# Kernel optimization log

Hardware: AMD Instinct MI355X
Metric: run time of the kernel (lower is better)

## Reference

```python
import jax, jax.numpy as jnp
import numpy as np

DPSI_THRESHOLD = 0.05
MSE_WEIGHT = 10.0
LOGIT_EPS = 1e-7
N = 8192


def setup_inputs() -> dict:
    key = jax.random.key(0)
    k1, k2 = jax.random.split(key)
    pred_psi_val = jax.random.normal(k1, (N,), dtype=jnp.float32)
    psi_val = jax.random.uniform(k2, (N,), dtype=jnp.float32)
    return {"pred_psi_val": pred_psi_val, "psi_val": psi_val, "use_BCE_loss_only": 0}


def _bce_with_logits(logits, targets):
    # numerically stable BCE-with-logits, mean reduction
    return jnp.mean(jnp.maximum(logits, 0.0) - logits * targets
                    + jnp.log1p(jnp.exp(-jnp.abs(logits))))


def _logit(p, eps):
    # torch.special.logit(p, eps): clamp p to [eps, 1-eps] then log(p/(1-p))
    p = jnp.clip(p, eps, 1.0 - eps)
    return jnp.log(p) - jnp.log1p(-p)


def reference(pred_psi_val, psi_val, use_BCE_loss_only):
    loss = _bce_with_logits(pred_psi_val, psi_val)
    if use_BCE_loss_only:  # static python flag
        return loss
    psi_logit = _logit(psi_val, LOGIT_EPS)
    # all-pairs differences [N, N]
    pred_diff = pred_psi_val[:, None] - pred_psi_val[None, :]
    true_diff = psi_logit[:, None] - psi_logit[None, :]
    ori_true_diff = psi_val[:, None] - psi_val[None, :]
    valid = jnp.abs(ori_true_diff) >= DPSI_THRESHOLD
    n_valid = jnp.sum(valid)
    sq = jnp.where(valid, (pred_diff - true_diff) ** 2, 0.0)
    pairwise_mse = jnp.sum(sq) / jnp.maximum(n_valid, 1).astype(sq.dtype)
    # add pairwise term only if at least one valid pair exists
    return jnp.where(n_valid > 0, loss + MSE_WEIGHT * pairwise_mse, loss)
```

## Files before the change

kernel.cpp:

```cpp
#include <hip/hip_runtime.h>


constexpr float DPSI_T    = 0.05f;
constexpr float LOGIT_EPS = 1e-7f;
constexpr int   CB  = 128;
constexpr int   RPT = 4;
constexpr int   TPB = 256;

__device__ __forceinline__ float logit_f(float p) {
    p = fminf(fmaxf(p, LOGIT_EPS), 1.0f - LOGIT_EPS);
    return logf(p) - log1pf(-p);
}

__global__ __launch_bounds__(256) void pair_kernel(const float* __restrict__ pred,
                                                   const float* __restrict__ psi,
                                                   float* __restrict__ part_sum,
                                                   unsigned int* __restrict__ part_cnt,
                                                   float* __restrict__ part_bce,
                                                   int n) {
    __shared__ float2 tile[CB];
    const int tid = threadIdx.x;
    const float NANF = __int_as_float(0x7fc00000);
    const int slot = blockIdx.x * gridDim.y + blockIdx.y;

    if (tid < CB) {
        int j = blockIdx.y * CB + tid;
        if (j < n) {
            float pj = psi[j];
            tile[tid] = make_float2(pj, pred[j] - logit_f(pj));
        } else {
            tile[tid] = make_float2(NANF, 0.0f);
        }
    }

    float bce = 0.0f;
    if (tid < 16) {
        int i = slot * 16 + tid;
        if (i < n) {
            float x = pred[i], t = psi[i];
            bce = fmaxf(x, 0.0f) - x * t + log1pf(expf(-fabsf(x)));
        }
    }

    float psi_i[RPT], d_i[RPT];
    const int rbase = blockIdx.x * (TPB * RPT);
    #pragma unroll
    for (int r = 0; r < RPT; ++r) {
        int i = rbase + r * TPB + tid;
        if (i < n) {
            float pi = psi[i];
            psi_i[r] = pi;
            d_i[r]   = pred[i] - logit_f(pi);
        } else {
            psi_i[r] = NANF;
            d_i[r]   = 0.0f;
        }
    }
    __syncthreads();

    float sum[RPT] = {0.0f, 0.0f, 0.0f, 0.0f};
    unsigned int cntw = 0;
    #pragma unroll 8
    for (int k = 0; k < CB; ++k) {
        float2 t = tile[k];
        #pragma unroll
        for (int r = 0; r < RPT; ++r) {
            float dpsi = psi_i[r] - t.x;
            bool  v    = fabsf(dpsi) >= DPSI_T;
            float dd   = d_i[r] - t.y;
            float ddm  = v ? dd : 0.0f;
            sum[r] = fmaf(ddm, ddm, sum[r]);
            cntw += (unsigned int)__popcll(__ballot(v));
        }
    }

    float s = (sum[0] + sum[1]) + (sum[2] + sum[3]);
    for (int off = 32; off; off >>= 1) {
        s   += __shfl_down(s, off);
        bce += __shfl_down(bce, off);
    }

    __shared__ float wsum[4];
    __shared__ unsigned int wcnt[4];
    int wave = tid >> 6, lane = tid & 63;
    if (lane == 0) { wsum[wave] = s; wcnt[wave] = cntw; }
    __syncthreads();
    if (tid == 0) {
        float st = (wsum[0] + wsum[1]) + (wsum[2] + wsum[3]);
        unsigned int ct = wcnt[0] + wcnt[1] + wcnt[2] + wcnt[3];
        part_sum[slot] = st;
        part_cnt[slot] = ct;
        part_bce[slot] = bce;
    }
}

__global__ __launch_bounds__(256) void finalize_kernel(const int* __restrict__ flag,
                                                       const float* __restrict__ part_sum,
                                                       const unsigned int* __restrict__ part_cnt,
                                                       const float* __restrict__ part_bce,
                                                       int nparts,
                                                       float* __restrict__ out,
                                                       int n) {
    const int tid = threadIdx.x;

    float s = 0.0f, b = 0.0f;
    unsigned long long c = 0;
    for (int p = tid; p < nparts; p += 256) {
        s += part_sum[p];
        b += part_bce[p];
        c += (unsigned long long)part_cnt[p];
    }

    for (int off = 32; off; off >>= 1) {
        s += __shfl_down(s, off);
        b += __shfl_down(b, off);
        c += __shfl_down(c, off);
    }
    __shared__ float s4[4], b4[4];
    __shared__ unsigned long long c4[4];
    int wave = tid >> 6, lane = tid & 63;
    if (lane == 0) { s4[wave] = s; b4[wave] = b; c4[wave] = c; }
    __syncthreads();
    if (tid == 0) {
        float s_total = (s4[0] + s4[1]) + (s4[2] + s4[3]);
        float b_total = (b4[0] + b4[1]) + (b4[2] + b4[3]);
        unsigned long long c_total = c4[0] + c4[1] + c4[2] + c4[3];
        float loss = b_total / (float)n;
        if (flag[0] == 0 && c_total > 0) {
            loss += 10.0f * (s_total / (float)c_total);
        }
        out[0] = loss;
    }
}

extern "C" void kernel_launch(void* const* d_in, const int* in_sizes, int n_in,
                              void* d_out, int out_size, void* d_ws, size_t ws_size,
                              hipStream_t stream) {
    const float* pred = (const float*)d_in[0];
    const float* psi  = (const float*)d_in[1];
    const int*   flag = (const int*)d_in[2];
    float* out = (float*)d_out;
    int n = in_sizes[0];

    int nbr = (n + TPB * RPT - 1) / (TPB * RPT);
    int nbc = (n + CB - 1) / CB;
    int nparts = nbr * nbc;
    float* part_sum        = (float*)d_ws;
    unsigned int* part_cnt = (unsigned int*)((char*)d_ws + (size_t)nparts * sizeof(float));
    float* part_bce        = (float*)((char*)d_ws + (size_t)2 * nparts * sizeof(float));

    dim3 grid(nbr, nbc);
    pair_kernel<<<grid, TPB, 0, stream>>>(pred, psi, part_sum, part_cnt, part_bce, n);
    finalize_kernel<<<1, 256, 0, stream>>>(flag, part_sum, part_cnt, part_bce, nparts, out, n);
}
```

Before: 70.80 us.

## Exploit pair symmetry with triangular tiling and fuse finalize via grid sync

```diff
diff --git a/kernel.cpp b/kernel.cpp
--- a/kernel.cpp
+++ b/kernel.cpp
@@ -1,30 +1,45 @@
 #include <hip/hip_runtime.h>
+#include <hip/hip_cooperative_groups.h>
 
+
+namespace cg = cooperative_groups;
 
 constexpr float DPSI_T    = 0.05f;
 constexpr float LOGIT_EPS = 1e-7f;
 constexpr int   CB  = 128;
-constexpr int   RPT = 4;
+constexpr int   RB  = 256;
 constexpr int   TPB = 256;
+constexpr int   NRB = 32;
+constexpr int   NTILES = 1056;
 
 __device__ __forceinline__ float logit_f(float p) {
     p = fminf(fmaxf(p, LOGIT_EPS), 1.0f - LOGIT_EPS);
     return logf(p) - log1pf(-p);
 }
 
-__global__ __launch_bounds__(256) void pair_kernel(const float* __restrict__ pred,
-                                                   const float* __restrict__ psi,
-                                                   float* __restrict__ part_sum,
-                                                   unsigned int* __restrict__ part_cnt,
-                                                   float* __restrict__ part_bce,
-                                                   int n) {
+__device__ __forceinline__ int tri_off(int rb) { return rb * (65 - rb); }
+
+__global__ __launch_bounds__(256) void fused_kernel(const float* __restrict__ pred,
+                                                    const float* __restrict__ psi,
+                                                    const int* __restrict__ flag,
+                                                    float* __restrict__ part_sum,
+                                                    unsigned int* __restrict__ part_cnt,
+                                                    float* __restrict__ part_bce,
+                                                    float* __restrict__ out,
+                                                    int n) {
     __shared__ float2 tile[CB];
     const int tid = threadIdx.x;
+    const int t   = blockIdx.x;
     const float NANF = __int_as_float(0x7fc00000);
-    const int slot = blockIdx.x * gridDim.y + blockIdx.y;
+
+    int rb = (int)((65.0f - sqrtf(4225.0f - 4.0f * (float)t)) * 0.5f);
+    rb = max(0, min(NRB - 1, rb));
+    while (rb + 1 < NRB && tri_off(rb + 1) <= t) ++rb;
+    while (rb > 0 && tri_off(rb) > t) --rb;
+    const int cb = 2 * rb + (t - tri_off(rb));
 
     if (tid < CB) {
-        int j = blockIdx.y * CB + tid;
+        int j = cb * CB + tid;
         if (j < n) {
             float pj = psi[j];
             tile[tid] = make_float2(pj, pred[j] - logit_f(pj));
@@ -34,102 +49,89 @@
     }
 
     float bce = 0.0f;
-    if (tid < 16) {
-        int i = slot * 16 + tid;
-        if (i < n) {
-            float x = pred[i], t = psi[i];
-            bce = fmaxf(x, 0.0f) - x * t + log1pf(expf(-fabsf(x)));
+    if (tid < 8) {
+        int i = t * 8 + tid;
+        if (t < 1024 && i < n) {
+            float x = pred[i], tt = psi[i];
+            bce = fmaxf(x, 0.0f) - x * tt + log1pf(expf(-fabsf(x)));
         }
     }
 
-    float psi_i[RPT], d_i[RPT];
-    const int rbase = blockIdx.x * (TPB * RPT);
-    #pragma unroll
-    for (int r = 0; r < RPT; ++r) {
-        int i = rbase + r * TPB + tid;
+    float psi_i, d_i;
+    {
+        int i = rb * RB + tid;
         if (i < n) {
             float pi = psi[i];
-            psi_i[r] = pi;
-            d_i[r]   = pred[i] - logit_f(pi);
+            psi_i = pi;
+            d_i   = pred[i] - logit_f(pi);
         } else {
-            psi_i[r] = NANF;
-            d_i[r]   = 0.0f;
+            psi_i = NANF;
+            d_i   = 0.0f;
         }
     }
     __syncthreads();
 
-    float sum[RPT] = {0.0f, 0.0f, 0.0f, 0.0f};
+    const int base = cb * CB - rb * RB;
+
+    float sum = 0.0f;
     unsigned int cntw = 0;
     #pragma unroll 8
     for (int k = 0; k < CB; ++k) {
-        float2 t = tile[k];
-        #pragma unroll
-        for (int r = 0; r < RPT; ++r) {
-            float dpsi = psi_i[r] - t.x;
-            bool  v    = fabsf(dpsi) >= DPSI_T;
-            float dd   = d_i[r] - t.y;
-            float ddm  = v ? dd : 0.0f;
-            sum[r] = fmaf(ddm, ddm, sum[r]);
-            cntw += (unsigned int)__popcll(__ballot(v));
-        }
+        float2 tc = tile[k];
+        float dpsi = psi_i - tc.x;
+        bool  v    = (fabsf(dpsi) >= DPSI_T) && (base + k > tid);
+        float dd   = d_i - tc.y;
+        float ddm  = v ? dd : 0.0f;
+        sum = fmaf(ddm, ddm, sum);
+        cntw += (unsigned int)__popcll(__ballot(v));
     }
 
-    float s = (sum[0] + sum[1]) + (sum[2] + sum[3]);
     for (int off = 32; off; off >>= 1) {
-        s   += __shfl_down(s, off);
+        sum += __shfl_down(sum, off);
         bce += __shfl_down(bce, off);
     }
 
     __shared__ float wsum[4];
     __shared__ unsigned int wcnt[4];
     int wave = tid >> 6, lane = tid & 63;
-    if (lane == 0) { wsum[wave] = s; wcnt[wave] = cntw; }
+    if (lane == 0) { wsum[wave] = sum; wcnt[wave] = cntw; }
     __syncthreads();
     if (tid == 0) {
-        float st = (wsum[0] + wsum[1]) + (wsum[2] + wsum[3]);
-        unsigned int ct = wcnt[0] + wcnt[1] + wcnt[2] + wcnt[3];
-        part_sum[slot] = st;
-        part_cnt[slot] = ct;
-        part_bce[slot] = bce;
+        part_sum[t] = (wsum[0] + wsum[1]) + (wsum[2] + wsum[3]);
+        part_cnt[t] = wcnt[0] + wcnt[1] + wcnt[2] + wcnt[3];
+        part_bce[t] = bce;
     }
-}
+    __threadfence();
 
-__global__ __launch_bounds__(256) void finalize_kernel(const int* __restrict__ flag,
-                                                       const float* __restrict__ part_sum,
-                                                       const unsigned int* __restrict__ part_cnt,
-                                                       const float* __restrict__ part_bce,
-                                                       int nparts,
-                                                       float* __restrict__ out,
-                                                       int n) {
-    const int tid = threadIdx.x;
+    cg::this_grid().sync();
 
-    float s = 0.0f, b = 0.0f;
-    unsigned long long c = 0;
-    for (int p = tid; p < nparts; p += 256) {
-        s += part_sum[p];
-        b += part_bce[p];
-        c += (unsigned long long)part_cnt[p];
-    }
-
-    for (int off = 32; off; off >>= 1) {
-        s += __shfl_down(s, off);
-        b += __shfl_down(b, off);
-        c += __shfl_down(c, off);
-    }
-    __shared__ float s4[4], b4[4];
-    __shared__ unsigned long long c4[4];
-    int wave = tid >> 6, lane = tid & 63;
-    if (lane == 0) { s4[wave] = s; b4[wave] = b; c4[wave] = c; }
-    __syncthreads();
-    if (tid == 0) {
-        float s_total = (s4[0] + s4[1]) + (s4[2] + s4[3]);
-        float b_total = (b4[0] + b4[1]) + (b4[2] + b4[3]);
-        unsigned long long c_total = c4[0] + c4[1] + c4[2] + c4[3];
-        float loss = b_total / (float)n;
-        if (flag[0] == 0 && c_total > 0) {
-            loss += 10.0f * (s_total / (float)c_total);
+    if (blockIdx.x == 0) {
+        float s = 0.0f, b = 0.0f;
+        unsigned long long c = 0;
+        for (int p = tid; p < NTILES; p += TPB) {
+            s += part_sum[p];
+            b += part_bce[p];
+            c += (unsigned long long)part_cnt[p];
         }
-        out[0] = loss;
+        for (int off = 32; off; off >>= 1) {
+            s += __shfl_down(s, off);
+            b += __shfl_down(b, off);
+            c += __shfl_down(c, off);
+        }
+        __shared__ float s4[4], b4[4];
+        __shared__ unsigned long long c4[4];
+        if (lane == 0) { s4[wave] = s; b4[wave] = b; c4[wave] = c; }
+        __syncthreads();
+        if (tid == 0) {
+            float s_total = (s4[0] + s4[1]) + (s4[2] + s4[3]);
+            float b_total = (b4[0] + b4[1]) + (b4[2] + b4[3]);
+            unsigned long long c_total = c4[0] + c4[1] + c4[2] + c4[3];
+            float loss = b_total / (float)n;
+            if (flag[0] == 0 && c_total > 0) {
+                loss += 10.0f * (s_total / (float)c_total);
+            }
+            out[0] = loss;
+        }
     }
 }
 
@@ -142,14 +144,12 @@
     float* out = (float*)d_out;
     int n = in_sizes[0];
 
-    int nbr = (n + TPB * RPT - 1) / (TPB * RPT);
-    int nbc = (n + CB - 1) / CB;
-    int nparts = nbr * nbc;
     float* part_sum        = (float*)d_ws;
-    unsigned int* part_cnt = (unsigned int*)((char*)d_ws + (size_t)nparts * sizeof(float));
-    float* part_bce        = (float*)((char*)d_ws + (size_t)2 * nparts * sizeof(float));
+    unsigned int* part_cnt = (unsigned int*)((char*)d_ws + (size_t)NTILES * sizeof(float));
+    float* part_bce        = (float*)((char*)d_ws + (size_t)2 * NTILES * sizeof(float));
 
-    dim3 grid(nbr, nbc);
-    pair_kernel<<<grid, TPB, 0, stream>>>(pred, psi, part_sum, part_cnt, part_bce, n);
-    finalize_kernel<<<1, 256, 0, stream>>>(flag, part_sum, part_cnt, part_bce, nparts, out, n);
+    void* args[] = {(void*)&pred, (void*)&psi, (void*)&flag, (void*)&part_sum,
+                    (void*)&part_cnt, (void*)&part_bce, (void*)&out, (void*)&n};
+    hipLaunchCooperativeKernel((const void*)fused_kernel, dim3(NTILES), dim3(TPB),
+                               args, 0, stream);
 }
```

Result: slower. 183.3 us (+158.9%).
